# Performance work log

Measured on AMD Instinct MI355X. Metric: run time of the kernel, lower is better.

## Reference

```python
import jax, jax.numpy as jnp
import numpy as np

EMBED = 512
HEADS = 8
HEAD_DIM = EMBED // HEADS


def setup_inputs() -> dict:
    key = jax.random.key(0)
    ks = jax.random.split(key, 7)
    N, Q, K = 8, 2048, 4096
    s = 1.0 / np.sqrt(EMBED)
    return {
        "x": jax.random.normal(ks[0], (N, Q, EMBED), dtype=jnp.float32),
        "y": jax.random.normal(ks[1], (N, K, EMBED), dtype=jnp.float32),
        "Wq": jax.random.normal(ks[2], (EMBED, EMBED), dtype=jnp.float32) * s,
        "Wk": jax.random.normal(ks[3], (EMBED, EMBED), dtype=jnp.float32) * s,
        "Wv": jax.random.normal(ks[4], (EMBED, EMBED), dtype=jnp.float32) * s,
        "Wo": jax.random.normal(ks[5], (EMBED, EMBED), dtype=jnp.float32) * s,
        "bo": jax.random.normal(ks[6], (EMBED,), dtype=jnp.float32) * 0.01,
    }


def reference(x, y, Wq, Wk, Wv, Wo, bo):
    N, Q, _ = x.shape
    K = y.shape[1]
    # torch Linear: out = in @ W.T
    queries = (x @ Wq.T).reshape(N, Q, HEADS, HEAD_DIM)
    keys = (y @ Wk.T).reshape(N, K, HEADS, HEAD_DIM)
    values = (y @ Wv.T).reshape(N, K, HEADS, HEAD_DIM)
    # NOTE: heads are SUMMED in the score einsum (head-collapsed attention)
    energy = jnp.einsum("nqhd,nkhd->nqk", queries, keys)  # [N,Q,K]
    attention = jax.nn.softmax(energy / jnp.sqrt(jnp.float32(EMBED)), axis=2)
    out = jnp.einsum("nqk,nkhd->nqhd", attention, values).reshape(N, Q, EMBED)
    return x + out @ Wo.T + bo
```

## Files before the change

### kernel.cpp

```cpp
#include <hip/hip_runtime.h>
#include <stdint.h>

typedef unsigned short u16;
typedef short bf16x8 __attribute__((ext_vector_type(8)));
typedef float f32x4 __attribute__((ext_vector_type(4)));
typedef u16 u16x8 __attribute__((ext_vector_type(8)));
typedef u16 u16x4v __attribute__((ext_vector_type(4)));
typedef uint32_t u32x4 __attribute__((ext_vector_type(4)));

#define EMBED 512
#define NBATCH 8
#define QLEN 2048
#define KLEN 4096

__device__ __forceinline__ u16 f2bf(float f) {
  uint32_t u = __builtin_bit_cast(uint32_t, f);
  u += 0x7fffu + ((u >> 16) & 1u);
  return (u16)(u >> 16);
}
__device__ __forceinline__ float bf2f(u16 b) {
  return __builtin_bit_cast(float, (uint32_t)b << 16);
}

__device__ __forceinline__ void gload_lds16(const void* g, void* lds) {
  __builtin_amdgcn_global_load_lds(
      (__attribute__((address_space(1))) void*)(uintptr_t)g,
      (__attribute__((address_space(3))) void*)(uint32_t)(uintptr_t)lds,
      16, 0, 0);
}

__global__ __launch_bounds__(256) void cvt_all_kernel(
    const float* __restrict__ x, const float* __restrict__ y,
    const float* __restrict__ wq, const float* __restrict__ wk,
    const float* __restrict__ wv, const float* __restrict__ wo,
    u16* __restrict__ dst) {
  const int64_t B0 = 2097152;
  const int64_t B1 = B0 + 4194304;
  const int64_t B2 = B1 + 65536;
  const int64_t B3 = B2 + 65536;
  const int64_t B4 = B3 + 65536;
  int64_t i = (int64_t)blockIdx.x * 256 + threadIdx.x;
  const float* src; int64_t off;
  if (i < B0)      { src = x;  off = 0;  }
  else if (i < B1) { src = y;  off = B0; }
  else if (i < B2) { src = wq; off = B1; }
  else if (i < B3) { src = wk; off = B2; }
  else if (i < B4) { src = wv; off = B3; }
  else             { src = wo; off = B4; }
  float4 f = ((const float4*)src)[i - off];
  u16x4v o = { f2bf(f.x), f2bf(f.y), f2bf(f.z), f2bf(f.w) };
  ((u16x4v*)dst)[i] = o;
}

constexpr int EPI_BF16 = 0;
constexpr int EPI_BF16_SCALE = 1;
constexpr int EPI_BF16_TRANS = 2;
constexpr int EPI_F32_RESID = 3;

template <int MODE>
__global__ __launch_bounds__(256, 2) void gemm_bt(
    const u16* __restrict__ A, const u16* __restrict__ B, void* __restrict__ Cv,
    int M, int N, int K,
    int64_t aBatch, int64_t bBatch, int64_t cBatch,
    float scale, const float* __restrict__ xres, const float* __restrict__ bias,
    u16* __restrict__ Vt) {
  __shared__ __align__(16) u16 As[128 * 64];
  __shared__ __align__(16) u16 Bs[128 * 64];

  const int tid = threadIdx.x;
  const int wave = tid >> 6;
  const int lane = tid & 63;
  const int bz = blockIdx.z;
  const int row0 = blockIdx.x * 128;
  const int col0 = blockIdx.y * 128;
  const u16* Ab = A + (int64_t)bz * aBatch;
  const u16* Bb = B + (int64_t)bz * bBatch;

  const int srow = wave * 32 + (lane >> 3);
  const int scol = (lane & 7) * 8;
  const u16* aSrc = Ab + (int64_t)(row0 + srow) * K + scol;
  const u16* bSrc = Bb + (int64_t)(col0 + srow) * K + scol;

  const int wm = (wave >> 1) * 64;
  const int wn = (wave & 1) * 64;
  const int fr = lane & 15;
  const int fq = lane >> 4;

  f32x4 acc[4][4];
#pragma unroll
  for (int mi = 0; mi < 4; ++mi)
#pragma unroll
    for (int ni = 0; ni < 4; ++ni) acc[mi][ni] = 0.0f;

  const int nkt = K >> 6;
  for (int kt = 0; kt < nkt; ++kt) {
    __syncthreads();
    const u16* aS = aSrc + kt * 64;
    const u16* bS = bSrc + kt * 64;
#pragma unroll
    for (int i = 0; i < 4; ++i) {
      gload_lds16(aS + (int64_t)(i * 8) * K, &As[(wave * 32 + i * 8) * 64]);
      gload_lds16(bS + (int64_t)(i * 8) * K, &Bs[(wave * 32 + i * 8) * 64]);
    }
    __syncthreads();
#pragma unroll
    for (int ks = 0; ks < 2; ++ks) {
      bf16x8 af[4], bfr[4];
#pragma unroll
      for (int mi = 0; mi < 4; ++mi)
        af[mi] = *(const bf16x8*)&As[(wm + mi * 16 + fr) * 64 + ks * 32 + fq * 8];
#pragma unroll
      for (int ni = 0; ni < 4; ++ni)
        bfr[ni] = *(const bf16x8*)&Bs[(wn + ni * 16 + fr) * 64 + ks * 32 + fq * 8];
#pragma unroll
      for (int mi = 0; mi < 4; ++mi)
#pragma unroll
        for (int ni = 0; ni < 4; ++ni)
          acc[mi][ni] = __builtin_amdgcn_mfma_f32_16x16x32_bf16(af[mi], bfr[ni],
                                                                acc[mi][ni], 0, 0, 0);
    }
  }

  if constexpr (MODE == EPI_BF16 || MODE == EPI_BF16_SCALE) {
    u16* C = (u16*)Cv + (int64_t)bz * cBatch;
#pragma unroll
    for (int mi = 0; mi < 4; ++mi) {
      const int rowb = row0 + wm + mi * 16 + fq * 4;
#pragma unroll
      for (int ni = 0; ni < 4; ++ni) {
        const int col = col0 + wn + ni * 16 + fr;
#pragma unroll
        for (int r = 0; r < 4; ++r) {
          float v = acc[mi][ni][r];
          if constexpr (MODE == EPI_BF16_SCALE) v *= scale;
          C[(int64_t)(rowb + r) * N + col] = f2bf(v);
        }
      }
    }
  } else if constexpr (MODE == EPI_BF16_TRANS) {
#pragma unroll
    for (int mi = 0; mi < 4; ++mi) {
      const int rowb = row0 + wm + mi * 16 + fq * 4;
      const int nb = rowb >> 12;
      const int kk = rowb & 4095;
#pragma unroll
      for (int ni = 0; ni < 4; ++ni) {
        const int col = col0 + wn + ni * 16 + fr;
        u16x4v o = { f2bf(acc[mi][ni][0]), f2bf(acc[mi][ni][1]),
                     f2bf(acc[mi][ni][2]), f2bf(acc[mi][ni][3]) };
        *(u16x4v*)&Vt[((int64_t)nb * EMBED + col) * KLEN + kk] = o;
      }
    }
  } else {
    float* C = (float*)Cv;
#pragma unroll
    for (int mi = 0; mi < 4; ++mi) {
      const int rowb = row0 + wm + mi * 16 + fq * 4;
#pragma unroll
      for (int ni = 0; ni < 4; ++ni) {
        const int col = col0 + wn + ni * 16 + fr;
        const float bv = bias[col];
#pragma unroll
        for (int r = 0; r < 4; ++r) {
          const int64_t idx = (int64_t)(rowb + r) * N + col;
          C[idx] = acc[mi][ni][r] + xres[idx] + bv;
        }
      }
    }
  }
}

__global__ __launch_bounds__(256, 1) void attn_kernel(
    const u16* __restrict__ Qm, const u16* __restrict__ Km,
    const u16* __restrict__ Vt, u16* __restrict__ O) {
  __shared__ __align__(16) u16 Ks[2][32 * 512];
  __shared__ __align__(16) u16 Vs[2][512 * 32];

  const int tid = threadIdx.x;
  const int w = tid >> 6;
  const int lane = tid & 63;
  const int fr = lane & 15, fq = lane >> 4;
  const int s7 = fr & 7;
  const int nb = blockIdx.x & 7;
  const int qt = blockIdx.x >> 3;

  bf16x8 q[16];
  {
    const u16* Qb = Qm + ((int64_t)nb * QLEN + qt * 64 + w * 16 + fr) * EMBED + fq * 8;
#pragma unroll
    for (int kc = 0; kc < 16; ++kc) q[kc] = *(const bf16x8*)&Qb[kc * 32];
  }

  f32x4 o[32];
#pragma unroll
  for (int i = 0; i < 32; ++i) o[i] = 0.0f;
  float mrun = -1e30f, lrun = 0.0f;

  const u16* Kb = Km + (int64_t)nb * KLEN * EMBED;
  const u16* Vb = Vt + (int64_t)nb * (int64_t)EMBED * KLEN;

  const int vrow = lane >> 2;
  const int vcl = (lane & 3) ^ ((lane >> 3) & 3);
  const int vswz = ((fr >> 1) & 3);

  {
    const u16* srcK = Kb + (int64_t)(w * 8) * EMBED;
#pragma unroll
    for (int i = 0; i < 8; ++i)
      gload_lds16(srcK + (int64_t)i * EMBED + (lane ^ i) * 8, &Ks[0][(w * 8 + i) * 512]);
#pragma unroll
    for (int i = 0; i < 8; ++i) {
      const int row0 = w * 128 + i * 16;
      gload_lds16(Vb + (int64_t)(row0 + vrow) * KLEN + vcl * 8, &Vs[0][row0 * 32]);
    }
  }
  __syncthreads();

  const int NT = KLEN / 32;
  for (int t = 0; t < NT; ++t) {
    const int cur = t & 1;
    if (t + 1 < NT) {
      const u16* srcK = Kb + ((int64_t)(t + 1) * 32 + w * 8) * EMBED;
#pragma unroll
      for (int i = 0; i < 8; ++i)
        gload_lds16(srcK + (int64_t)i * EMBED + (lane ^ i) * 8,
                    &Ks[cur ^ 1][(w * 8 + i) * 512]);
#pragma unroll
      for (int i = 0; i < 8; ++i) {
        const int row0 = w * 128 + i * 16;
        gload_lds16(Vb + (int64_t)(row0 + vrow) * KLEN + (t + 1) * 32 + vcl * 8,
                    &Vs[cur ^ 1][row0 * 32]);
      }
    }

    const u16* Kc = Ks[cur];
    f32x4 s0 = 0.0f, s1 = 0.0f;
#pragma unroll
    for (int kc = 0; kc < 16; ++kc) {
      bf16x8 k0 = *(const bf16x8*)&Kc[(fr)*512 + (((kc * 4 + fq) ^ s7) * 8)];
      bf16x8 k1 = *(const bf16x8*)&Kc[(16 + fr) * 512 + (((kc * 4 + fq) ^ s7) * 8)];
      s0 = __builtin_amdgcn_mfma_f32_16x16x32_bf16(k0, q[kc], s0, 0, 0, 0);
      s1 = __builtin_amdgcn_mfma_f32_16x16x32_bf16(k1, q[kc], s1, 0, 0, 0);
    }

    const u16* Vc = Vs[cur];
    bf16x8 vA[16];
#pragma unroll
    for (int dt = 0; dt < 16; ++dt)
      vA[dt] = *(const bf16x8*)&Vc[(dt * 16 + fr) * 32 + ((fq ^ vswz) * 8)];

    float mt = fmaxf(fmaxf(fmaxf(s0[0], s0[1]), fmaxf(s0[2], s0[3])),
                     fmaxf(fmaxf(s1[0], s1[1]), fmaxf(s1[2], s1[3])));
    mt = fmaxf(mt, __shfl_xor(mt, 16));
    mt = fmaxf(mt, __shfl_xor(mt, 32));
    float alpha = 1.0f;
    if (!__all(mt <= mrun + 8.0f)) {
      const float mn = fmaxf(mrun, mt);
      alpha = __expf(mrun - mn);
      lrun *= alpha;
      mrun = mn;
    }
    float p0[4], p1[4];
    float rs = 0.0f;
#pragma unroll
    for (int r = 0; r < 4; ++r) {
      p0[r] = __expf(s0[r] - mrun);
      p1[r] = __expf(s1[r] - mrun);
      rs += p0[r] + p1[r];
    }
    rs += __shfl_xor(rs, 16);
    rs += __shfl_xor(rs, 32);
    lrun += rs;

    const uint32_t lo0 = (uint32_t)f2bf(p0[0]) | ((uint32_t)f2bf(p0[1]) << 16);
    const uint32_t lo1 = (uint32_t)f2bf(p0[2]) | ((uint32_t)f2bf(p0[3]) << 16);
    const uint32_t hi0 = (uint32_t)f2bf(p1[0]) | ((uint32_t)f2bf(p1[1]) << 16);
    const uint32_t hi1 = (uint32_t)f2bf(p1[2]) | ((uint32_t)f2bf(p1[3]) << 16);
    const int srcA = fr + (((fq << 1) & 3) << 4);
    const int srcB = srcA + 16;
    const bool useHi = (fq >= 2);
    const uint32_t aLo0 = __shfl(lo0, srcA), aHi0 = __shfl(hi0, srcA);
    const uint32_t aLo1 = __shfl(lo1, srcA), aHi1 = __shfl(hi1, srcA);
    const uint32_t bLo0 = __shfl(lo0, srcB), bHi0 = __shfl(hi0, srcB);
    const uint32_t bLo1 = __shfl(lo1, srcB), bHi1 = __shfl(hi1, srcB);
    u32x4 pd;
    pd[0] = useHi ? aHi0 : aLo0;
    pd[1] = useHi ? aHi1 : aLo1;
    pd[2] = useHi ? bHi0 : bLo0;
    pd[3] = useHi ? bHi1 : bLo1;
    const bf16x8 pb = __builtin_bit_cast(bf16x8, pd);

    if (__any(alpha != 1.0f)) {
      float ra[4];
#pragma unroll
      for (int r = 0; r < 4; ++r) ra[r] = __shfl(alpha, (fq << 2) + r);
#pragma unroll
      for (int dt = 0; dt < 32; ++dt)
#pragma unroll
        for (int r = 0; r < 4; ++r) o[dt][r] *= ra[r];
    }

    bf16x8 vB[16];
#pragma unroll
    for (int dt = 0; dt < 16; ++dt)
      vB[dt] = *(const bf16x8*)&Vc[((16 + dt) * 16 + fr) * 32 + ((fq ^ vswz) * 8)];

#pragma unroll
    for (int dt = 0; dt < 16; ++dt)
      o[dt] = __builtin_amdgcn_mfma_f32_16x16x32_bf16(pb, vA[dt], o[dt], 0, 0, 0);
#pragma unroll
    for (int dt = 0; dt < 16; ++dt)
      o[16 + dt] = __builtin_amdgcn_mfma_f32_16x16x32_bf16(pb, vB[dt], o[16 + dt],
                                                           0, 0, 0);

    __syncthreads();
  }

  float linv[4];
#pragma unroll
  for (int r = 0; r < 4; ++r) linv[r] = 1.0f / __shfl(lrun, (fq << 2) + r);
  u16* Ob = O + ((int64_t)nb * QLEN + qt * 64 + w * 16) * EMBED;
#pragma unroll
  for (int dt = 0; dt < 32; ++dt)
#pragma unroll
    for (int r = 0; r < 4; ++r)
      Ob[(int64_t)((fq << 2) + r) * EMBED + dt * 16 + fr] = f2bf(o[dt][r] * linv[r]);
}

extern "C" void kernel_launch(void* const* d_in, const int* in_sizes, int n_in,
                              void* d_out, int out_size, void* d_ws, size_t ws_size,
                              hipStream_t stream) {
  const float* x  = (const float*)d_in[0];
  const float* y  = (const float*)d_in[1];
  const float* Wq = (const float*)d_in[2];
  const float* Wk = (const float*)d_in[3];
  const float* Wv = (const float*)d_in[4];
  const float* Wo = (const float*)d_in[5];
  const float* bo = (const float*)d_in[6];
  float* out = (float*)d_out;

  const int64_t nx = (int64_t)NBATCH * QLEN * EMBED;
  const int64_t ny = (int64_t)NBATCH * KLEN * EMBED;
  const int64_t nw = (int64_t)EMBED * EMBED;

  u16* w   = (u16*)d_ws;
  u16* xb  = w;
  u16* O   = w; w += nx;
  u16* yb  = w; w += ny;
  u16* Wqb = w; w += nw;
  u16* Wkb = w; w += nw;
  u16* Wvb = w; w += nw;
  u16* Wob = w; w += nw;
  u16* Qm  = w; w += nx;
  u16* Km  = w; w += ny;
  u16* Vt  = w; w += ny;

  cvt_all_kernel<<<25600, 256, 0, stream>>>(x, y, Wq, Wk, Wv, Wo, xb);

  const float scal = 0.04419417382415922f;
  gemm_bt<EPI_BF16_SCALE><<<dim3(128, 4, 1), 256, 0, stream>>>(
      xb, Wqb, Qm, 16384, EMBED, EMBED, 0, 0, 0, scal, nullptr, nullptr, nullptr);
  gemm_bt<EPI_BF16><<<dim3(256, 4, 1), 256, 0, stream>>>(
      yb, Wkb, Km, 32768, EMBED, EMBED, 0, 0, 0, 1.f, nullptr, nullptr, nullptr);
  gemm_bt<EPI_BF16_TRANS><<<dim3(256, 4, 1), 256, 0, stream>>>(
      yb, Wvb, nullptr, 32768, EMBED, EMBED, 0, 0, 0, 1.f, nullptr, nullptr, Vt);

  attn_kernel<<<NBATCH * 32, 256, 0, stream>>>(Qm, Km, Vt, O);

  gemm_bt<EPI_F32_RESID><<<dim3(128, 4, 1), 256, 0, stream>>>(
      O, Wob, out, 16384, EMBED, EMBED, 0, 0, 0, 1.f, x, bo, nullptr);
}
```

Measured before the change: 409.3 us.

## Store V in MFMA-fragment order and load it directly from global memory

The V projection epilogue now writes V in a tiled, fragment-ready layout, so each lane's MFMA B operand is one contiguous 16-byte chunk. The attention kernel drops the LDS double buffer for V and loads V fragments straight from global memory into registers each iteration. This removes the V LDS traffic and frees shared memory. In exchange, global load latency now sits in the inner loop without async staging, and every wavefront re-reads the same V data through cache instead of sharing it in LDS.

```diff
diff --git a/kernel.cpp b/kernel.cpp
--- a/kernel.cpp
+++ b/kernel.cpp
@@ -143,12 +143,18 @@
       const int rowb = row0 + wm + mi * 16 + fq * 4;
       const int nb = rowb >> 12;
       const int kk = rowb & 4095;
+      const int tt = kk >> 5;
+      const int kq = (kk >> 3) & 3;
+      const int ke = kk & 7;
 #pragma unroll
       for (int ni = 0; ni < 4; ++ni) {
         const int col = col0 + wn + ni * 16 + fr;
+        const int dt = col >> 4;
+        const int dr = col & 15;
         u16x4v o = { f2bf(acc[mi][ni][0]), f2bf(acc[mi][ni][1]),
                      f2bf(acc[mi][ni][2]), f2bf(acc[mi][ni][3]) };
-        *(u16x4v*)&Vt[((int64_t)nb * EMBED + col) * KLEN + kk] = o;
+        *(u16x4v*)&Vt[(((int64_t)nb * 128 + tt) * 32 + dt) * 512 +
+                      (kq * 16 + dr) * 8 + ke] = o;
       }
     }
   } else {
@@ -172,9 +178,8 @@
 
 __global__ __launch_bounds__(256, 1) void attn_kernel(
     const u16* __restrict__ Qm, const u16* __restrict__ Km,
-    const u16* __restrict__ Vt, u16* __restrict__ O) {
+    const u16* __restrict__ Vf, u16* __restrict__ O) {
   __shared__ __align__(16) u16 Ks[2][32 * 512];
-  __shared__ __align__(16) u16 Vs[2][512 * 32];
 
   const int tid = threadIdx.x;
   const int w = tid >> 6;
@@ -197,22 +202,13 @@
   float mrun = -1e30f, lrun = 0.0f;
 
   const u16* Kb = Km + (int64_t)nb * KLEN * EMBED;
-  const u16* Vb = Vt + (int64_t)nb * (int64_t)EMBED * KLEN;
-
-  const int vrow = lane >> 2;
-  const int vcl = (lane & 3) ^ ((lane >> 3) & 3);
-  const int vswz = ((fr >> 1) & 3);
+  const u16* Vb = Vf + (int64_t)nb * 128 * 32 * 512 + lane * 8;
 
   {
     const u16* srcK = Kb + (int64_t)(w * 8) * EMBED;
 #pragma unroll
     for (int i = 0; i < 8; ++i)
       gload_lds16(srcK + (int64_t)i * EMBED + (lane ^ i) * 8, &Ks[0][(w * 8 + i) * 512]);
-#pragma unroll
-    for (int i = 0; i < 8; ++i) {
-      const int row0 = w * 128 + i * 16;
-      gload_lds16(Vb + (int64_t)(row0 + vrow) * KLEN + vcl * 8, &Vs[0][row0 * 32]);
-    }
   }
   __syncthreads();
 
@@ -225,13 +221,12 @@
       for (int i = 0; i < 8; ++i)
         gload_lds16(srcK + (int64_t)i * EMBED + (lane ^ i) * 8,
                     &Ks[cur ^ 1][(w * 8 + i) * 512]);
-#pragma unroll
-      for (int i = 0; i < 8; ++i) {
-        const int row0 = w * 128 + i * 16;
-        gload_lds16(Vb + (int64_t)(row0 + vrow) * KLEN + (t + 1) * 32 + vcl * 8,
-                    &Vs[cur ^ 1][row0 * 32]);
-      }
-    }
+    }
+
+    bf16x8 vA[16];
+#pragma unroll
+    for (int dt = 0; dt < 16; ++dt)
+      vA[dt] = *(const bf16x8*)&Vb[((int64_t)t * 32 + dt) * 512];
 
     const u16* Kc = Ks[cur];
     f32x4 s0 = 0.0f, s1 = 0.0f;
@@ -242,12 +237,6 @@
       s0 = __builtin_amdgcn_mfma_f32_16x16x32_bf16(k0, q[kc], s0, 0, 0, 0);
       s1 = __builtin_amdgcn_mfma_f32_16x16x32_bf16(k1, q[kc], s1, 0, 0, 0);
     }
-
-    const u16* Vc = Vs[cur];
-    bf16x8 vA[16];
-#pragma unroll
-    for (int dt = 0; dt < 16; ++dt)
-      vA[dt] = *(const bf16x8*)&Vc[(dt * 16 + fr) * 32 + ((fq ^ vswz) * 8)];
 
     float mt = fmaxf(fmaxf(fmaxf(s0[0], s0[1]), fmaxf(s0[2], s0[3])),
                      fmaxf(fmaxf(s1[0], s1[1]), fmaxf(s1[2], s1[3])));
@@ -271,6 +260,11 @@
     rs += __shfl_xor(rs, 16);
     rs += __shfl_xor(rs, 32);
     lrun += rs;
+
+    bf16x8 vB[16];
+#pragma unroll
+    for (int dt = 0; dt < 16; ++dt)
+      vB[dt] = *(const bf16x8*)&Vb[((int64_t)t * 32 + 16 + dt) * 512];
 
     const uint32_t lo0 = (uint32_t)f2bf(p0[0]) | ((uint32_t)f2bf(p0[1]) << 16);
     const uint32_t lo1 = (uint32_t)f2bf(p0[2]) | ((uint32_t)f2bf(p0[3]) << 16);
@@ -300,11 +294,6 @@
         for (int r = 0; r < 4; ++r) o[dt][r] *= ra[r];
     }
 
-    bf16x8 vB[16];
-#pragma unroll
-    for (int dt = 0; dt < 16; ++dt)
-      vB[dt] = *(const bf16x8*)&Vc[((16 + dt) * 16 + fr) * 32 + ((fq ^ vswz) * 8)];
-
 #pragma unroll
     for (int dt = 0; dt < 16; ++dt)
       o[dt] = __builtin_amdgcn_mfma_f32_16x16x32_bf16(pb, vA[dt], o[dt], 0, 0, 0);
```

New measurement: 665.0 us. +62.5%, slower.
